# Optimization experiments

Hardware: AMD Instinct MI355X
Metric: run time of the kernel (lower is better)

## Reference

```python
import jax, jax.numpy as jnp
import numpy as np
import math

N_HEAD = 4
NORM_GROUPS = 32
EPS = 1e-5

def setup_inputs() -> dict:
    key = jax.random.key(0)
    k1, k2, k3 = jax.random.split(key, 3)
    B, C, H, W = 2, 256, 64, 64
    x = jax.random.normal(k1, (B, C, H, W), dtype=jnp.float32)
    gamma = jnp.ones((C,), dtype=jnp.float32)
    beta = jnp.zeros((C,), dtype=jnp.float32)
    w_qkv = jax.random.normal(k2, (3 * C, C), dtype=jnp.float32) / math.sqrt(C)
    w_out = jax.random.normal(k3, (C, C), dtype=jnp.float32) / math.sqrt(C)
    b_out = jnp.zeros((C,), dtype=jnp.float32)
    return {"x": x, "gamma": gamma, "beta": beta, "w_qkv": w_qkv, "w_out": w_out, "b_out": b_out}

def group_norm(x, gamma, beta):
    B, C, H, W = x.shape
    g = x.reshape(B, NORM_GROUPS, C // NORM_GROUPS, H, W)
    mean = g.mean(axis=(2, 3, 4), keepdims=True)
    var = g.var(axis=(2, 3, 4), keepdims=True)
    g = (g - mean) * jax.lax.rsqrt(var + EPS)
    return g.reshape(B, C, H, W) * gamma[None, :, None, None] + beta[None, :, None, None]

def reference(x, gamma, beta, w_qkv, w_out, b_out):
    B, C, H, W = x.shape
    S = H * W
    hd = C // N_HEAD  # head_dim
    normed = group_norm(x, gamma, beta)
    # 1x1 conv == channel matmul; flatten spatial to S
    qkv = jnp.einsum('oc,bcs->bos', w_qkv, normed.reshape(B, C, S))  # [B, 3C, S]
    qkv = qkv.reshape(B, N_HEAD, 3 * hd, S)
    q, k, v = jnp.split(qkv, 3, axis=2)  # each [B, N, hd, S]
    # note: original scales by sqrt(channel), NOT sqrt(head_dim)
    attn = jnp.einsum('bnds,bndt->bnst', q, k) / math.sqrt(C)  # [B, N, S, S]
    attn = jax.nn.softmax(attn, axis=-1)
    out = jnp.einsum('bnst,bndt->bnds', attn, v)  # [B, N, hd, S]
    out = out.reshape(B, C, S)
    out = jnp.einsum('oc,bcs->bos', w_out, out) + b_out[None, :, None]
    return out.reshape(B, C, H, W) + x
```

## Files before the change

### kernel.cpp

```cpp
#include <hip/hip_runtime.h>
#include <hip/hip_bf16.h>
#include <cstdint>
#include <cstddef>

#define SDIM 4096
#define CDIM 256
#define HSZ (64 * 4096)
#define POS ((size_t)2 * SDIM * CDIM)

typedef __attribute__((ext_vector_type(8))) short bf16x8;
typedef __attribute__((ext_vector_type(8))) __bf16 bfv8;
typedef __attribute__((ext_vector_type(4))) float f32x4;
typedef __attribute__((ext_vector_type(16))) float f32x16;

__device__ __forceinline__ float bf2f(short u) {
  union { uint32_t i; float f; } v; v.i = ((uint32_t)(uint16_t)u) << 16; return v.f;
}
__device__ __forceinline__ short bfc(float f) { return __builtin_bit_cast(short, (__bf16)f); }
__device__ __forceinline__ short4 pk4(float a, float b, float c, float d) {
  short4 r; r.x = bfc(a); r.y = bfc(b); r.z = bfc(c); r.w = bfc(d); return r;
}
__device__ __forceinline__ unsigned pkbf(float lo, float hi) {
  union { short s[2]; unsigned u; } r;
  r.s[0] = bfc(lo); r.s[1] = bfc(hi);
  return r.u;
}
__device__ __forceinline__ f32x4 MFMA(bf16x8 a, bf16x8 b, f32x4 c) {
  return __builtin_amdgcn_mfma_f32_16x16x32_bf16(
      __builtin_bit_cast(bfv8, a), __builtin_bit_cast(bfv8, b), c, 0, 0, 0);
}
__device__ __forceinline__ f32x16 MFMA32(bf16x8 a, bf16x8 b, f32x16 c) {
  return __builtin_amdgcn_mfma_f32_32x32x16_bf16(
      __builtin_bit_cast(bfv8, a), __builtin_bit_cast(bfv8, b), c, 0, 0, 0);
}

#define SCQ 0.09016844f

__global__ __launch_bounds__(256) void prep1_k(
    const float* __restrict__ x, const float* __restrict__ wq,
    const float* __restrict__ wo, float* __restrict__ gnws,
    short* __restrict__ wqb, short* __restrict__ wob) {
  __shared__ float red[8];
  int blk = blockIdx.x;
  int tid = threadIdx.x;
  if (blk < 512) {
    const float4* xv = (const float4*)(x + (size_t)(blk >> 3) * 32768 + (blk & 7) * 4096);
    float sum = 0.f, sq = 0.f;
#pragma unroll
    for (int i = 0; i < 4; ++i) {
      float4 v = xv[tid + i * 256];
      sum += (v.x + v.y) + (v.z + v.w);
      sq += (v.x * v.x + v.y * v.y) + (v.z * v.z + v.w * v.w);
    }
#pragma unroll
    for (int m = 1; m < 64; m <<= 1) {
      sum += __shfl_xor(sum, m);
      sq += __shfl_xor(sq, m);
    }
    if ((tid & 63) == 0) { red[(tid >> 6) * 2] = sum; red[(tid >> 6) * 2 + 1] = sq; }
    __syncthreads();
    if (tid == 0) {
      gnws[blk * 2] = red[0] + red[2] + red[4] + red[6];
      gnws[blk * 2 + 1] = red[1] + red[3] + red[5] + red[7];
    }
  } else {
    int i = (blk - 512) * 256 + tid;
    if (i < 49152) {
      float4 v = ((const float4*)wq)[i];
      ((short4*)wqb)[i] = pk4(v.x, v.y, v.z, v.w);
    } else {
      float4 v = ((const float4*)wo)[i - 49152];
      ((short4*)wob)[i - 49152] = pk4(v.x, v.y, v.z, v.w);
    }
  }
}

__global__ __launch_bounds__(256) void gemm_qkv(const short* __restrict__ W,
                                                const float* __restrict__ x,
                                                const float* __restrict__ gnws,
                                                const float* __restrict__ gamma,
                                                const float* __restrict__ beta,
                                                short* __restrict__ qkv) {
  constexpr int XS = 264;
  __shared__ short xs[64 * XS];
  __shared__ float ga_s[256], be_s[256];
  int blk = blockIdx.x;
  int xcd = blk & 7;
  int rem = blk >> 3;
  int n = rem & 3;
  int tile = (rem >> 2) * 8 + xcd;
  int by = tile & 63;
  int bz = tile >> 6;
  int tid = threadIdx.x;

  {
    int c = tid;
    int g = c >> 3;
    const float* gw = gnws + (size_t)(bz * 32 + g) * 16;
    float sum = 0.f, sq = 0.f;
#pragma unroll
    for (int k = 0; k < 8; ++k) { sum += gw[k * 2]; sq += gw[k * 2 + 1]; }
    float mean = sum * (1.f / 32768.f);
    float var = sq * (1.f / 32768.f) - mean * mean;
    float rstd = rsqrtf(var + 1e-5f);
    float ga = gamma[c] * rstd;
    ga_s[c] = ga;
    be_s[c] = beta[c] - mean * ga;
  }
  __syncthreads();

  {
    int s_loc = tid & 63;
    const float* xb = x + (size_t)bz * 256 * SDIM + by * 64 + s_loc;
#pragma unroll
    for (int it = 0; it < 8; ++it) {
      int c0 = ((tid >> 6) + it * 4) * 8;
      float v[8];
#pragma unroll
      for (int j = 0; j < 8; ++j)
        v[j] = xb[(size_t)(c0 + j) * SDIM] * ga_s[c0 + j] + be_s[c0 + j];
      union { short4 h[2]; bf16x8 v8; } o;
      o.h[0] = pk4(v[0], v[1], v[2], v[3]);
      o.h[1] = pk4(v[4], v[5], v[6], v[7]);
      *(bf16x8*)(xs + s_loc * XS + c0) = o.v8;
    }
  }
  __syncthreads();

  int w = tid >> 6, lane = tid & 63;
  int sl = lane & 15, kg = lane >> 4;
  const short* Wq = W + (size_t)(n * 192 + w * 16 + sl) * CDIM + kg * 8;
  const short* Wk = Wq + (size_t)64 * CDIM;
  const short* Wv = Wq + (size_t)128 * CDIM;
  f32x4 zero = {0.f, 0.f, 0.f, 0.f};
  f32x4 accq[4] = {zero, zero, zero, zero};
  f32x4 acck[4] = {zero, zero, zero, zero};
  f32x4 accv[4] = {zero, zero, zero, zero};
#pragma unroll
  for (int kk = 0; kk < 8; ++kk) {
    bf16x8 aq = *(const bf16x8*)(Wq + kk * 32);
    bf16x8 ak = *(const bf16x8*)(Wk + kk * 32);
    bf16x8 av = *(const bf16x8*)(Wv + kk * 32);
#pragma unroll
    for (int nb = 0; nb < 4; ++nb) {
      bf16x8 bfr = *(const bf16x8*)(xs + (nb * 16 + sl) * XS + kk * 32 + kg * 8);
      accq[nb] = MFMA(aq, bfr, accq[nb]);
      acck[nb] = MFMA(ak, bfr, acck[nb]);
      accv[nb] = MFMA(av, bfr, accv[nb]);
    }
  }
  size_t hbase = (size_t)(bz * 4 + n) * 3 * HSZ;
  short* qt = qkv + hbase;
  short* kt = qkv + hbase + HSZ;
  short* vp = qkv + hbase + 2 * HSZ;
#pragma unroll
  for (int nb = 0; nb < 4; ++nb) {
    int s = by * 64 + nb * 16 + sl;
    *(short4*)(qt + (size_t)s * 64 + w * 16 + kg * 4) =
        pk4(accq[nb][0] * SCQ, accq[nb][1] * SCQ, accq[nb][2] * SCQ, accq[nb][3] * SCQ);
    *(short4*)(kt + (size_t)s * 64 + w * 16 + kg * 4) =
        pk4(acck[nb][0], acck[nb][1], acck[nb][2], acck[nb][3]);
#pragma unroll
    for (int r = 0; r < 4; ++r)
      vp[(size_t)(w * 16 + kg * 4 + r) * SDIM + s] = bfc(accv[nb][r]);
  }
}

#define ZERO16 {0.f,0.f,0.f,0.f,0.f,0.f,0.f,0.f,0.f,0.f,0.f,0.f,0.f,0.f,0.f,0.f}
#define TSTR 72
#define TILE (64 * TSTR)
#define BF1 ((short)0x3F80)
__global__ __launch_bounds__(512, 4) void attn_k(const short* __restrict__ qkv,
                                                 short* __restrict__ po,
                                                 float* __restrict__ pl) {
  __shared__ short smem[2 * 2 * TILE];

  int blk = blockIdx.x;
  int nb = blk & 7;
  int tb = (blk >> 3) & 3;
  int sblk = blk >> 5;
  int tid = threadIdx.x;
  int w = tid >> 6, lane = tid & 63;
  int l5 = lane & 31, h = lane >> 5;

  size_t hbase = (size_t)nb * 3 * HSZ;
  const short* qt = qkv + hbase;
  const short* kt = qkv + hbase + HSZ;
  const short* vp = qkv + hbase + 2 * HSZ;

  int s0w = sblk * 256 + w * 32;

  bf16x8 qf[4];
#pragma unroll
  for (int kc = 0; kc < 4; ++kc)
    qf[kc] = *(const bf16x8*)(qt + (size_t)(s0w + l5) * 64 + kc * 16 + h * 8);

  const bf16x8 ones = {BF1, BF1, BF1, BF1, BF1, BF1, BF1, BF1};

  int srow = tid >> 3;
  int sch = tid & 7;
  int tbase = tb * 1024;

  bf16x8 kreg, vreg;
  kreg = *(const bf16x8*)(kt + (size_t)(tbase + srow) * 64 + sch * 8);
  vreg = *(const bf16x8*)(vp + (size_t)srow * SDIM + tbase + sch * 8);
  *(bf16x8*)(smem + srow * TSTR + sch * 8) = kreg;
  *(bf16x8*)(smem + TILE + srow * TSTR + sch * 8) = vreg;
  __syncthreads();

  f32x16 acc_o0 = ZERO16, acc_o1 = ZERO16, acc_l = ZERO16;

  for (int step = 0; step < 16; ++step) {
    short* kbuf = smem + (step & 1) * 2 * TILE;
    short* vbuf = kbuf + TILE;
    if (step + 1 < 16) {
      int t1 = tbase + (step + 1) * 64;
      kreg = *(const bf16x8*)(kt + (size_t)(t1 + srow) * 64 + sch * 8);
      vreg = *(const bf16x8*)(vp + (size_t)srow * SDIM + t1 + sch * 8);
    }

    f32x16 accs0 = ZERO16, accs1 = ZERO16;
#pragma unroll
    for (int kc = 0; kc < 4; ++kc) {
      bf16x8 k0 = *(const bf16x8*)(kbuf + l5 * TSTR + (kc * 2 + h) * 8);
      bf16x8 k1 = *(const bf16x8*)(kbuf + (32 + l5) * TSTR + (kc * 2 + h) * 8);
      accs0 = MFMA32(k0, qf[kc], accs0);
      accs1 = MFMA32(k1, qf[kc], accs1);
    }

    float p0[16], p1[16];
#pragma unroll
    for (int r = 0; r < 16; ++r) p0[r] = __builtin_amdgcn_exp2f(accs0[r]);
#pragma unroll
    for (int r = 0; r < 16; ++r) p1[r] = __builtin_amdgcn_exp2f(accs1[r]);

#define PV_TC(pp, tcb, tc)                                                        \
    {                                                                             \
      unsigned a0 = pkbf(pp[8 * tcb + 0], pp[8 * tcb + 1]);                       \
      unsigned a1 = pkbf(pp[8 * tcb + 2], pp[8 * tcb + 3]);                       \
      unsigned b0 = pkbf(pp[8 * tcb + 4], pp[8 * tcb + 5]);                       \
      unsigned b1 = pkbf(pp[8 * tcb + 6], pp[8 * tcb + 7]);                       \
      asm volatile("v_permlane32_swap_b32 %0, %1" : "+v"(a0), "+v"(b0));          \
      asm volatile("v_permlane32_swap_b32 %0, %1" : "+v"(a1), "+v"(b1));          \
      union { unsigned u[4]; bf16x8 v; } F;                                       \
      F.u[0] = a0; F.u[1] = a1; F.u[2] = b0; F.u[3] = b1;                         \
      int c8 = (tc * 2 + h) * 8;                                                  \
      bf16x8 v0 = *(const bf16x8*)(vbuf + l5 * TSTR + c8);                        \
      bf16x8 v1 = *(const bf16x8*)(vbuf + (32 + l5) * TSTR + c8);                 \
      acc_o0 = MFMA32(F.v, v0, acc_o0);                                           \
      acc_o1 = MFMA32(F.v, v1, acc_o1);                                           \
      acc_l = MFMA32(F.v, ones, acc_l);                                           \
    }
    PV_TC(p0, 0, 0)
    PV_TC(p0, 1, 1)
    PV_TC(p1, 0, 2)
    PV_TC(p1, 1, 3)
#undef PV_TC

    if (step + 1 < 16) {
      short* kn = smem + ((step + 1) & 1) * 2 * TILE;
      *(bf16x8*)(kn + srow * TSTR + sch * 8) = kreg;
      *(bf16x8*)(kn + TILE + srow * TSTR + sch * 8) = vreg;
    }
    __syncthreads();
  }

  if (l5 == 0) {
    float* plp = pl + ((size_t)tb * 8 + nb) * SDIM + s0w;
#pragma unroll
    for (int r = 0; r < 16; ++r) {
      int srw = (r & 3) + 8 * (r >> 2) + 4 * h;
      plp[srw] = acc_l[r];
    }
  }
  int n = nb & 3, b = nb >> 2;
#pragma unroll
  for (int r = 0; r < 16; ++r) {
    int srw = (r & 3) + 8 * (r >> 2) + 4 * h;
    int sg = s0w + srw;
    size_t rowb = ((size_t)(tb * 2 + b) * SDIM + sg) * CDIM + n * 64;
    po[rowb + l5] = bfc(acc_o0[r]);
    po[rowb + 32 + l5] = bfc(acc_o1[r]);
  }
}

__global__ __launch_bounds__(512) void gemm_out(const short* __restrict__ po,
                                                const float* __restrict__ pl,
                                                const short* __restrict__ WO,
                                                const float* __restrict__ bias,
                                                const float* __restrict__ resid,
                                                float* __restrict__ out) {
  constexpr int AS = 264;
  __shared__ short als[32 * AS];
  int by = blockIdx.x;
  int bz = blockIdx.y;
  int tid = threadIdx.x;
  {
    int row = tid >> 4;
    int c0 = (tid & 15) * 16;
    int srow = by * 32 + row;
    int n = c0 >> 6;
    float l = 0.f;
#pragma unroll
    for (int t = 0; t < 4; ++t) l += pl[(size_t)(t * 8 + bz * 4 + n) * SDIM + srow];
    float inv = 1.f / l;
    const short* Ap = po + ((size_t)bz * SDIM + srow) * CDIM + c0;
    float f[16];
#pragma unroll
    for (int j = 0; j < 16; ++j) f[j] = 0.f;
#pragma unroll
    for (int t = 0; t < 4; ++t) {
      bf16x8 u0 = *(const bf16x8*)(Ap + t * POS);
      bf16x8 u1 = *(const bf16x8*)(Ap + t * POS + 8);
#pragma unroll
      for (int j = 0; j < 8; ++j) { f[j] += bf2f(u0[j]); f[8 + j] += bf2f(u1[j]); }
    }
    union { unsigned u[4]; bf16x8 v; } o0, o1;
#pragma unroll
    for (int j = 0; j < 4; ++j) {
      o0.u[j] = pkbf(f[2 * j] * inv, f[2 * j + 1] * inv);
      o1.u[j] = pkbf(f[8 + 2 * j] * inv, f[9 + 2 * j] * inv);
    }
    *(bf16x8*)(als + row * AS + c0) = o0.v;
    *(bf16x8*)(als + row * AS + c0 + 8) = o1.v;
  }
  __syncthreads();
  int w = tid >> 6, lane = tid & 63;
  int l5 = lane & 31, h = lane >> 5;
  const short* Wr = WO + (size_t)(w * 32 + l5) * CDIM + h * 8;
  f32x16 acc = ZERO16;
#pragma unroll
  for (int kk = 0; kk < 16; ++kk) {
    bf16x8 wf = *(const bf16x8*)(Wr + kk * 16);
    bf16x8 af = *(const bf16x8*)(als + l5 * AS + kk * 16 + h * 8);
    acc = MFMA32(wf, af, acc);
  }
  int s = by * 32 + l5;
#pragma unroll
  for (int r = 0; r < 16; ++r) {
    int ol = (r & 3) + 8 * (r >> 2) + 4 * h;
    int o = w * 32 + ol;
    size_t idx = ((size_t)bz * CDIM + o) * SDIM + s;
    out[idx] = acc[r] + bias[o] + resid[idx];
  }
}

extern "C" void kernel_launch(void* const* d_in, const int* in_sizes, int n_in,
                              void* d_out, int out_size, void* d_ws, size_t ws_size,
                              hipStream_t stream) {
  const float* x = (const float*)d_in[0];
  const float* gamma = (const float*)d_in[1];
  const float* beta = (const float*)d_in[2];
  const float* wqkv = (const float*)d_in[3];
  const float* wout = (const float*)d_in[4];
  const float* bout = (const float*)d_in[5];
  float* out = (float*)d_out;

  short* wq_bf = (short*)d_ws;
  short* wo_bf = wq_bf + 768 * 256;
  short* qkvb = wo_bf + 256 * 256;
  short* po = qkvb + (size_t)2 * 768 * SDIM;
  float* pl = (float*)(po + 4 * POS);
  float* gnws = pl + 4 * 8 * SDIM;

  hipLaunchKernelGGL(prep1_k, dim3(768), dim3(256), 0, stream, x, wqkv, wout, gnws,
                     wq_bf, wo_bf);
  hipLaunchKernelGGL(gemm_qkv, dim3(512), dim3(256), 0, stream, wq_bf, x, gnws,
                     gamma, beta, qkvb);
  hipLaunchKernelGGL(attn_k, dim3(512), dim3(512), 0, stream, qkvb, po, pl);
  hipLaunchKernelGGL(gemm_out, dim3(128, 2), dim3(512), 0, stream, po, pl, wo_bf,
                     bout, x, out);
}
```

Measured before the change: 69.81 us.

## Give each attention wave 64 query rows to reuse K/V LDS fragments

```diff
diff --git a/kernel.cpp b/kernel.cpp
--- a/kernel.cpp
+++ b/kernel.cpp
@@ -170,7 +170,7 @@
 #define TSTR 72
 #define TILE (64 * TSTR)
 #define BF1 ((short)0x3F80)
-__global__ __launch_bounds__(512, 4) void attn_k(const short* __restrict__ qkv,
+__global__ __launch_bounds__(256, 2) void attn_k(const short* __restrict__ qkv,
                                                  short* __restrict__ po,
                                                  float* __restrict__ pl) {
   __shared__ short smem[2 * 2 * TILE];
@@ -188,79 +188,106 @@
   const short* kt = qkv + hbase + HSZ;
   const short* vp = qkv + hbase + 2 * HSZ;
 
-  int s0w = sblk * 256 + w * 32;
-
-  bf16x8 qf[4];
-#pragma unroll
-  for (int kc = 0; kc < 4; ++kc)
-    qf[kc] = *(const bf16x8*)(qt + (size_t)(s0w + l5) * 64 + kc * 16 + h * 8);
+  int s0w = sblk * 256 + w * 64;
+
+  bf16x8 qf0[4], qf1[4];
+#pragma unroll
+  for (int kc = 0; kc < 4; ++kc) {
+    qf0[kc] = *(const bf16x8*)(qt + (size_t)(s0w + l5) * 64 + kc * 16 + h * 8);
+    qf1[kc] = *(const bf16x8*)(qt + (size_t)(s0w + 32 + l5) * 64 + kc * 16 + h * 8);
+  }
 
   const bf16x8 ones = {BF1, BF1, BF1, BF1, BF1, BF1, BF1, BF1};
 
-  int srow = tid >> 3;
-  int sch = tid & 7;
+  int srow = tid >> 2;
+  int sc16 = (tid & 3) * 16;
   int tbase = tb * 1024;
 
-  bf16x8 kreg, vreg;
-  kreg = *(const bf16x8*)(kt + (size_t)(tbase + srow) * 64 + sch * 8);
-  vreg = *(const bf16x8*)(vp + (size_t)srow * SDIM + tbase + sch * 8);
-  *(bf16x8*)(smem + srow * TSTR + sch * 8) = kreg;
-  *(bf16x8*)(smem + TILE + srow * TSTR + sch * 8) = vreg;
+  bf16x8 kreg0, kreg1, vreg0, vreg1;
+  kreg0 = *(const bf16x8*)(kt + (size_t)(tbase + srow) * 64 + sc16);
+  kreg1 = *(const bf16x8*)(kt + (size_t)(tbase + srow) * 64 + sc16 + 8);
+  vreg0 = *(const bf16x8*)(vp + (size_t)srow * SDIM + tbase + sc16);
+  vreg1 = *(const bf16x8*)(vp + (size_t)srow * SDIM + tbase + sc16 + 8);
+  *(bf16x8*)(smem + srow * TSTR + sc16) = kreg0;
+  *(bf16x8*)(smem + srow * TSTR + sc16 + 8) = kreg1;
+  *(bf16x8*)(smem + TILE + srow * TSTR + sc16) = vreg0;
+  *(bf16x8*)(smem + TILE + srow * TSTR + sc16 + 8) = vreg1;
   __syncthreads();
 
-  f32x16 acc_o0 = ZERO16, acc_o1 = ZERO16, acc_l = ZERO16;
+  f32x16 o00 = ZERO16, o01 = ZERO16, o10 = ZERO16, o11 = ZERO16;
+  f32x16 l0 = ZERO16, l1 = ZERO16;
 
   for (int step = 0; step < 16; ++step) {
     short* kbuf = smem + (step & 1) * 2 * TILE;
     short* vbuf = kbuf + TILE;
     if (step + 1 < 16) {
       int t1 = tbase + (step + 1) * 64;
-      kreg = *(const bf16x8*)(kt + (size_t)(t1 + srow) * 64 + sch * 8);
-      vreg = *(const bf16x8*)(vp + (size_t)srow * SDIM + t1 + sch * 8);
-    }
-
-    f32x16 accs0 = ZERO16, accs1 = ZERO16;
+      kreg0 = *(const bf16x8*)(kt + (size_t)(t1 + srow) * 64 + sc16);
+      kreg1 = *(const bf16x8*)(kt + (size_t)(t1 + srow) * 64 + sc16 + 8);
+      vreg0 = *(const bf16x8*)(vp + (size_t)srow * SDIM + t1 + sc16);
+      vreg1 = *(const bf16x8*)(vp + (size_t)srow * SDIM + t1 + sc16 + 8);
+    }
+
+    f32x16 a00 = ZERO16, a01 = ZERO16, a10 = ZERO16, a11 = ZERO16;
 #pragma unroll
     for (int kc = 0; kc < 4; ++kc) {
       bf16x8 k0 = *(const bf16x8*)(kbuf + l5 * TSTR + (kc * 2 + h) * 8);
       bf16x8 k1 = *(const bf16x8*)(kbuf + (32 + l5) * TSTR + (kc * 2 + h) * 8);
-      accs0 = MFMA32(k0, qf[kc], accs0);
-      accs1 = MFMA32(k1, qf[kc], accs1);
-    }
-
-    float p0[16], p1[16];
-#pragma unroll
-    for (int r = 0; r < 16; ++r) p0[r] = __builtin_amdgcn_exp2f(accs0[r]);
-#pragma unroll
-    for (int r = 0; r < 16; ++r) p1[r] = __builtin_amdgcn_exp2f(accs1[r]);
-
-#define PV_TC(pp, tcb, tc)                                                        \
+      a00 = MFMA32(k0, qf0[kc], a00);
+      a01 = MFMA32(k0, qf1[kc], a01);
+      a10 = MFMA32(k1, qf0[kc], a10);
+      a11 = MFMA32(k1, qf1[kc], a11);
+    }
+
+#pragma unroll
+    for (int r = 0; r < 16; ++r) a00[r] = __builtin_amdgcn_exp2f(a00[r]);
+#pragma unroll
+    for (int r = 0; r < 16; ++r) a01[r] = __builtin_amdgcn_exp2f(a01[r]);
+#pragma unroll
+    for (int r = 0; r < 16; ++r) a10[r] = __builtin_amdgcn_exp2f(a10[r]);
+#pragma unroll
+    for (int r = 0; r < 16; ++r) a11[r] = __builtin_amdgcn_exp2f(a11[r]);
+
+#define PV_TC(pa, pb, tcb, tc)                                                    \
     {                                                                             \
-      unsigned a0 = pkbf(pp[8 * tcb + 0], pp[8 * tcb + 1]);                       \
-      unsigned a1 = pkbf(pp[8 * tcb + 2], pp[8 * tcb + 3]);                       \
-      unsigned b0 = pkbf(pp[8 * tcb + 4], pp[8 * tcb + 5]);                       \
-      unsigned b1 = pkbf(pp[8 * tcb + 6], pp[8 * tcb + 7]);                       \
+      unsigned a0 = pkbf(pa[8 * tcb + 0], pa[8 * tcb + 1]);                       \
+      unsigned a1 = pkbf(pa[8 * tcb + 2], pa[8 * tcb + 3]);                       \
+      unsigned b0 = pkbf(pa[8 * tcb + 4], pa[8 * tcb + 5]);                       \
+      unsigned b1 = pkbf(pa[8 * tcb + 6], pa[8 * tcb + 7]);                       \
       asm volatile("v_permlane32_swap_b32 %0, %1" : "+v"(a0), "+v"(b0));          \
       asm volatile("v_permlane32_swap_b32 %0, %1" : "+v"(a1), "+v"(b1));          \
-      union { unsigned u[4]; bf16x8 v; } F;                                       \
-      F.u[0] = a0; F.u[1] = a1; F.u[2] = b0; F.u[3] = b1;                         \
+      union { unsigned u[4]; bf16x8 v; } F0;                                      \
+      F0.u[0] = a0; F0.u[1] = a1; F0.u[2] = b0; F0.u[3] = b1;                     \
+      unsigned c0 = pkbf(pb[8 * tcb + 0], pb[8 * tcb + 1]);                       \
+      unsigned c1 = pkbf(pb[8 * tcb + 2], pb[8 * tcb + 3]);                       \
+      unsigned d0 = pkbf(pb[8 * tcb + 4], pb[8 * tcb + 5]);                       \
+      unsigned d1 = pkbf(pb[8 * tcb + 6], pb[8 * tcb + 7]);                       \
+      asm volatile("v_permlane32_swap_b32 %0, %1" : "+v"(c0), "+v"(d0));          \
+      asm volatile("v_permlane32_swap_b32 %0, %1" : "+v"(c1), "+v"(d1));          \
+      union { unsigned u[4]; bf16x8 v; } F1;                                      \
+      F1.u[0] = c0; F1.u[1] = c1; F1.u[2] = d0; F1.u[3] = d1;                     \
       int c8 = (tc * 2 + h) * 8;                                                  \
       bf16x8 v0 = *(const bf16x8*)(vbuf + l5 * TSTR + c8);                        \
       bf16x8 v1 = *(const bf16x8*)(vbuf + (32 + l5) * TSTR + c8);                 \
-      acc_o0 = MFMA32(F.v, v0, acc_o0);                                           \
-      acc_o1 = MFMA32(F.v, v1, acc_o1);                                           \
-      acc_l = MFMA32(F.v, ones, acc_l);                                           \
-    }
-    PV_TC(p0, 0, 0)
-    PV_TC(p0, 1, 1)
-    PV_TC(p1, 0, 2)
-    PV_TC(p1, 1, 3)
+      o00 = MFMA32(F0.v, v0, o00);                                                \
+      o01 = MFMA32(F0.v, v1, o01);                                                \
+      o10 = MFMA32(F1.v, v0, o10);                                                \
+      o11 = MFMA32(F1.v, v1, o11);                                                \
+      l0 = MFMA32(F0.v, ones, l0);                                                \
+      l1 = MFMA32(F1.v, ones, l1);                                                \
+    }
+    PV_TC(a00, a01, 0, 0)
+    PV_TC(a00, a01, 1, 1)
+    PV_TC(a10, a11, 0, 2)
+    PV_TC(a10, a11, 1, 3)
 #undef PV_TC
 
     if (step + 1 < 16) {
       short* kn = smem + ((step + 1) & 1) * 2 * TILE;
-      *(bf16x8*)(kn + srow * TSTR + sch * 8) = kreg;
-      *(bf16x8*)(kn + TILE + srow * TSTR + sch * 8) = vreg;
+      *(bf16x8*)(kn + srow * TSTR + sc16) = kreg0;
+      *(bf16x8*)(kn + srow * TSTR + sc16 + 8) = kreg1;
+      *(bf16x8*)(kn + TILE + srow * TSTR + sc16) = vreg0;
+      *(bf16x8*)(kn + TILE + srow * TSTR + sc16 + 8) = vreg1;
     }
     __syncthreads();
   }
@@ -270,17 +297,20 @@
 #pragma unroll
     for (int r = 0; r < 16; ++r) {
       int srw = (r & 3) + 8 * (r >> 2) + 4 * h;
-      plp[srw] = acc_l[r];
+      plp[srw] = l0[r];
+      plp[32 + srw] = l1[r];
     }
   }
   int n = nb & 3, b = nb >> 2;
 #pragma unroll
   for (int r = 0; r < 16; ++r) {
     int srw = (r & 3) + 8 * (r >> 2) + 4 * h;
-    int sg = s0w + srw;
-    size_t rowb = ((size_t)(tb * 2 + b) * SDIM + sg) * CDIM + n * 64;
-    po[rowb + l5] = bfc(acc_o0[r]);
-    po[rowb + 32 + l5] = bfc(acc_o1[r]);
+    size_t rowb0 = ((size_t)(tb * 2 + b) * SDIM + s0w + srw) * CDIM + n * 64;
+    size_t rowb1 = ((size_t)(tb * 2 + b) * SDIM + s0w + 32 + srw) * CDIM + n * 64;
+    po[rowb0 + l5] = bfc(o00[r]);
+    po[rowb0 + 32 + l5] = bfc(o01[r]);
+    po[rowb1 + l5] = bfc(o10[r]);
+    po[rowb1 + 32 + l5] = bfc(o11[r]);
   }
 }
 
@@ -367,7 +397,7 @@
                      wq_bf, wo_bf);
   hipLaunchKernelGGL(gemm_qkv, dim3(512), dim3(256), 0, stream, wq_bf, x, gnws,
                      gamma, beta, qkvb);
-  hipLaunchKernelGGL(attn_k, dim3(512), dim3(512), 0, stream, qkvb, po, pl);
+  hipLaunchKernelGGL(attn_k, dim3(512), dim3(256), 0, stream, qkvb, po, pl);
   hipLaunchKernelGGL(gemm_out, dim3(128, 2), dim3(512), 0, stream, po, pl, wo_bf,
                      bout, x, out);
 }
```

After: 70.42 us, median of 3. No clear change (+0.9%).
